# Kernel optimization log

Hardware: AMD Instinct MI355X
Metric: run time of the kernel (lower is better)

Reference implementation:

```python
import jax, jax.numpy as jnp
import numpy as np

DPITCH_RANGE = 24.0
SCALE = 1.0


def setup_inputs() -> dict:
    key = jax.random.key(0)
    ks = jax.random.split(key, 10)
    B, T, ND, SD, H = 512, 1024, 64, 3, 256
    inp_size = ND + SD  # 67
    w = lambda k, shape: (jax.random.normal(k, shape, jnp.float32) * 0.05)
    return {
        "noise": jax.random.normal(ks[0], (B, T, ND), jnp.float32),
        "gap_duration": jax.random.uniform(ks[1], (B, T + 1, SD - 1), dtype=jnp.float32),
        "W_ih": w(ks[2], (4 * H, inp_size)),
        "W_hh": w(ks[3], (4 * H, H)),
        "b_ih": w(ks[4], (4 * H,)),
        "b_hh": w(ks[5], (4 * H,)),
        "W1": w(ks[6], (H, H)),
        "b1": w(ks[7], (H,)),
        "W2": w(ks[8], (1, H)),
        "b2": w(ks[9], (1,)),
    }


def reference(noise, gap_duration, W_ih, W_hh, b_ih, b_hh, W1, b1, W2, b2):
    B, T, _ = noise.shape
    H = W_hh.shape[1]

    def head(out):  # Linear -> Tanh -> Linear -> Tanh, scaled to deltapitch
        hdn = jnp.tanh(out @ W1.T + b1)
        return jnp.tanh(hdn @ W2.T + b2) * (DPITCH_RANGE * SCALE)

    def lstm_cell(h, c, x):  # torch LSTM gate order: i, f, g, o
        gates = x @ W_ih.T + b_ih + h @ W_hh.T + b_hh
        i, f, g, o = jnp.split(gates, 4, axis=-1)
        c = jax.nn.sigmoid(f) * c + jax.nn.sigmoid(i) * jnp.tanh(g)
        h = jax.nn.sigmoid(o) * jnp.tanh(c)
        return h, c

    def step(carry, inp):
        out, h, c = carry
        n_t, gap_t = inp  # [B, ND], [B, SD-1]
        x = jnp.concatenate([gap_t, head(out)], axis=-1)  # [B, SD]
        h, c = lstm_cell(h, c, jnp.concatenate([x, n_t], axis=-1))
        return (h, h, c), x

    z = jnp.zeros((B, H), noise.dtype)
    (out, _, _), xs = jax.lax.scan(
        step, (z, z, z),
        (noise.transpose(1, 0, 2), gap_duration[:, :T].transpose(1, 0, 2)))
    x_last = jnp.concatenate([gap_duration[:, T], head(out)], axis=-1)
    return jnp.concatenate([xs.transpose(1, 0, 2), x_last[:, None, :]], axis=1)
```

## Files before the change

### kernel.cpp

```cpp
#include <hip/hip_runtime.h>
#include <stdint.h>
#include <stddef.h>

typedef __bf16 bf16x8 __attribute__((ext_vector_type(8)));
typedef float f32x4 __attribute__((ext_vector_type(4)));

#define MFMA16(a, b, c) __builtin_amdgcn_mfma_f32_16x16x32_bf16((a), (b), (c), 0, 0, 0)

#define TSTEPS 1024
#define NDIM   64
#define NKC    10
#define NGT    64
#define MB     16
#define GROUPS 32
#define SLICES 8

#define GOFF    ((size_t)0)
#define GBYTES  ((size_t)NGT * NKC * 1024)
#define W1OFF   (GOFF + GBYTES)
#define W1BYTES ((size_t)16 * 8 * 1024)
#define BOFF    (W1OFF + W1BYTES)
#define XOFF    (BOFF + 4096)
#define IDSB    ((size_t)1024)
#define PAYB    ((size_t)256 * 2 * 512 * 4)
#define WSNEED  (XOFF + IDSB + 2 * PAYB)

__device__ __forceinline__ uint16_t f2bf(float f) {
    union { float f; uint32_t u; } v; v.f = f;
    return (uint16_t)((v.u + 0x7FFFu + ((v.u >> 16) & 1u)) >> 16);
}
__device__ __forceinline__ float fsig(float x) { return 1.0f / (1.0f + __expf(-x)); }
__device__ __forceinline__ float ftanh(float x) { return 2.0f / (1.0f + __expf(-2.0f * x)) - 1.0f; }

__device__ __forceinline__ void bar_lgkm() {
    asm volatile("s_waitcnt lgkmcnt(0)" ::: "memory");
    __builtin_amdgcn_s_barrier();
    asm volatile("" ::: "memory");
}

#define FPOLL7(R0, R1, R2, R3, R4, R5, R6, O0, O1, O2, O3, O4, O5, O6, SB)   \
    asm volatile(                                                            \
        "global_load_dword %0, %7, %14 sc0\n\t"                              \
        "global_load_dword %1, %8, %14 sc0\n\t"                              \
        "global_load_dword %2, %9, %14 sc0\n\t"                              \
        "global_load_dword %3, %10, %14 sc0\n\t"                             \
        "global_load_dword %4, %11, %14 sc0\n\t"                             \
        "global_load_dword %5, %12, %14 sc0\n\t"                             \
        "global_load_dword %6, %13, %14 sc0\n\t"                             \
        "s_waitcnt vmcnt(0)"                                                 \
        : "=&v"(R0), "=&v"(R1), "=&v"(R2), "=&v"(R3),                        \
          "=&v"(R4), "=&v"(R5), "=&v"(R6)                                    \
        : "v"(O0), "v"(O1), "v"(O2), "v"(O3), "v"(O4), "v"(O5), "v"(O6),     \
          "s"(SB)                                                            \
        : "memory")

__global__ void prep_gates(const float* __restrict__ W_ih, const float* __restrict__ W_hh,
                           char* __restrict__ ws) {
    int F = blockIdx.x;
    int T = F / NKC, kc = F - T * NKC;
    int l = threadIdx.x;
    int row  = 16 * T + (l & 15);
    int unit = row >> 2, gt = row & 3;
    int orig = gt * 256 + unit;
    uint32_t w[4];
#pragma unroll
    for (int p = 0; p < 4; ++p) {
        float v[2];
#pragma unroll
        for (int e = 0; e < 2; ++e) {
            int k = 32 * kc + 8 * (l >> 4) + 2 * p + e;
            v[e] = (k < 64) ? W_ih[orig * 67 + 3 + k] : W_hh[orig * 256 + (k - 64)];
        }
        w[p] = (uint32_t)f2bf(v[0]) | ((uint32_t)f2bf(v[1]) << 16);
    }
    *(uint4*)(ws + GOFF + (size_t)F * 1024 + (size_t)l * 16) = make_uint4(w[0], w[1], w[2], w[3]);
}

__global__ void prep_w1(const float* __restrict__ W1, char* __restrict__ ws) {
    int F = blockIdx.x;
    int T = F / 8, kc = F - T * 8;
    int l = threadIdx.x;
    int row = 16 * T + (l & 15);
    uint32_t w[4];
#pragma unroll
    for (int p = 0; p < 4; ++p) {
        int k = 32 * kc + 8 * (l >> 4) + 2 * p;
        w[p] = (uint32_t)f2bf(W1[row * 256 + k]) | ((uint32_t)f2bf(W1[row * 256 + k + 1]) << 16);
    }
    *(uint4*)(ws + W1OFF + (size_t)F * 1024 + (size_t)l * 16) = make_uint4(w[0], w[1], w[2], w[3]);
}

__global__ void prep_small(const float* __restrict__ b_ih, const float* __restrict__ b_hh,
                           char* __restrict__ ws) {
    int t = threadIdx.x;
    float* sb = (float*)(ws + BOFF);
    if (t < 1024) {
        int unit = t >> 2, gt = t & 3;
        int orig = gt * 256 + unit;
        sb[t] = b_ih[orig] + b_hh[orig];
    }
}

__global__ __launch_bounds__(512, 2) void lstm_main(
        const float* __restrict__ noise, const float* __restrict__ gap,
        const float* __restrict__ W_ih, const float* __restrict__ b1p,
        const float* __restrict__ W2p, const float* __restrict__ b2p,
        char* __restrict__ ws, float* __restrict__ out) {
    __shared__ uint16_t act[MB * 320];
    __shared__ float dp_part[16][9];
    __shared__ float gxy[2][16][2];
    __shared__ int s_gf;

    const int tid  = threadIdx.x;
    const int w    = tid >> 6;
    const int lane = tid & 63;
    const int q    = lane >> 4;
    const int col  = lane & 15;
    const int g    = blockIdx.x >> 3;
    const int s    = blockIdx.x & 7;
    const int b0   = g * MB;
    const int swz  = (col & 7) << 3;

    const uint4* gfr  = (const uint4*)(ws + GOFF);
    const uint4* w1fr = (const uint4*)(ws + W1OFF);
    const float* bias = (const float*)(ws + BOFF);
    uint32_t* ids = (uint32_t*)(ws + XOFF);
    const uint64_t payF_base = (uint64_t)(uintptr_t)(ws + XOFF + IDSB);
    uint32_t* payS = (uint32_t*)(ws + XOFF + IDSB + PAYB);

    for (int i = tid; i < MB * 320; i += 512) act[i] = 0;

    const int T = 8 * s + w;
    uint4 gw[NKC];
#pragma unroll
    for (int kc = 0; kc < NKC; ++kc) gw[kc] = gfr[(size_t)(T * NKC + kc) * 64 + lane];
    uint4 w1w[16];
#pragma unroll
    for (int i = 0; i < 2; ++i)
#pragma unroll
        for (int kc = 0; kc < 8; ++kc)
            w1w[i * 8 + kc] = w1fr[(size_t)((2 * w + i) * 8 + kc) * 64 + lane];

    const int rb = 16 * T + 4 * q;
    const float bI = bias[rb], bF = bias[rb + 1], bG = bias[rb + 2], bO = bias[rb + 3];
    float wx0[4], wx1[4], wx2[4];
#pragma unroll
    for (int r = 0; r < 4; ++r) {
        int row = rb + r;
        int orig = (row & 3) * 256 + (row >> 2);
        wx0[r] = W_ih[orig * 67 + 0];
        wx1[r] = W_ih[orig * 67 + 1];
        wx2[r] = W_ih[orig * 67 + 2] * 24.0f;
    }
    float b1r[8], w2r[8];
#pragma unroll
    for (int a = 0; a < 2; ++a)
#pragma unroll
        for (int r = 0; r < 4; ++r) {
            int row = 32 * w + 16 * a + 4 * q + r;
            b1r[4 * a + r] = b1p[row];
            w2r[4 * a + r] = W2p[row];
        }
    const float b2v = b2p[0];

    const int myidx = g * 8 + s;
    const int myunit = 32 * s + 4 * w + q;

    uint32_t myx;
    asm volatile("s_getreg_b32 %0, hwreg(HW_REG_XCC_ID)" : "=s"(myx));
    if (tid == 0)
        __hip_atomic_store(&ids[myidx], 0x100u | (myx & 0xffu),
                           __ATOMIC_RELAXED, __HIP_MEMORY_SCOPE_AGENT);
    if (tid < 8) {
        uint32_t v;
        do { v = __hip_atomic_load(&ids[g * 8 + tid], __ATOMIC_RELAXED,
                                   __HIP_MEMORY_SCOPE_AGENT); } while (!(v & 0x100u));
        unsigned long long bal = __ballot((v & 0xffu) == (myx & 0xffu));
        if (tid == 0) s_gf = ((bal & 0xffull) == 0xffull) ? 1 : 0;
    }

    uint32_t vofB[7];
#pragma unroll
    for (int pi = 0; pi < 7; ++pi) {
        int p = (s + 1 + pi) & 7;
        vofB[pi] = ((uint32_t)(g * 8 + p) << 12) + (uint32_t)((64 * w + lane) * 4);
    }
    const uint32_t myvof = ((uint32_t)myidx << 12) + (uint32_t)((64 * w + lane) * 4);

    const int nbr = tid >> 5, nj = (tid & 31) * 2;
    const float* nptr = noise + (size_t)(b0 + nbr) * TSTEPS * NDIM + nj;
    float2 npf = *(const float2*)nptr;
    const bool xlead = (w == 7 && lane < 16);
    const bool olead = (s == 0 && w == 0);
    float2 gpf = make_float2(0.f, 0.f);
    if (xlead) gpf = *(const float2*)(gap + (size_t)(b0 + col) * (TSTEPS + 1) * 2);

    float creg = 0.f;
    float o_g0 = 0.f, o_g1 = 0.f, o_tdp = 0.f;
    const f32x4 fz = {0.f, 0.f, 0.f, 0.f};

    __syncthreads();
    bool fm = (s_gf != 0);

#pragma unroll 1
    for (int t = 0; t <= TSTEPS; ++t) {
        const int par = t & 1;
        const uint32_t tg = (uint32_t)t;

        if (t < TSTEPS) {
            uint32_t nv = (uint32_t)f2bf(npf.x) | ((uint32_t)f2bf(npf.y) << 16);
            int sw = (nbr & 7) << 3;
            *(uint32_t*)&act[nbr * 320 + (nj ^ sw)] = nv;
        }
        if (xlead) { gxy[par][col][0] = gpf.x; gxy[par][col][1] = gpf.y; }

        if (t > 0) {
            unsigned pend = 0x7f;
            if (fm) {
                int spins = 0;
                const uint32_t pb = (uint32_t)(par << 11);
                uint32_t o0 = vofB[0] + pb, o1 = vofB[1] + pb, o2 = vofB[2] + pb,
                         o3 = vofB[3] + pb, o4 = vofB[4] + pb, o5 = vofB[5] + pb,
                         o6 = vofB[6] + pb;
                for (;;) {
                    uint32_t r0, r1, r2, r3, r4, r5, r6;
                    FPOLL7(r0, r1, r2, r3, r4, r5, r6, o0, o1, o2, o3, o4, o5, o6,
                           payF_base);
                    uint32_t rr[7] = {r0, r1, r2, r3, r4, r5, r6};
#pragma unroll
                    for (int pi = 0; pi < 7; ++pi)
                        if ((pend & (1u << pi)) && (rr[pi] >> 16) == tg) {
                            int p = (s + 1 + pi) & 7;
                            int u = 32 * p + 4 * w + q;
                            act[col * 320 + ((64 + u) ^ swz)] = (uint16_t)rr[pi];
                            pend &= ~(1u << pi);
                        }
                    if (!pend) break;
                    if (++spins > 1000) { fm = false; break; }
                }
            }
            if (pend) {
                uint32_t vv[7];
                do {
#pragma unroll
                    for (int pi = 0; pi < 7; ++pi)
                        if (pend & (1u << pi)) {
                            int p = (s + 1 + pi) & 7;
                            vv[pi] = __hip_atomic_load(
                                &payS[(((g * 8 + p) * 2 + par) << 9) + 64 * w + lane],
                                __ATOMIC_RELAXED, __HIP_MEMORY_SCOPE_AGENT);
                        }
#pragma unroll
                    for (int pi = 0; pi < 7; ++pi)
                        if ((pend & (1u << pi)) && (vv[pi] >> 16) == tg) {
                            int p = (s + 1 + pi) & 7;
                            int u = 32 * p + 4 * w + q;
                            act[col * 320 + ((64 + u) ^ swz)] = (uint16_t)vv[pi];
                            pend &= ~(1u << pi);
                        }
                } while (pend);
            }
            fm = __all(fm);
            if (olead && q == 0) {
                float* o = out + ((size_t)(b0 + col) * (TSTEPS + 1) + (t - 1)) * 3;
                o[0] = o_g0; o[1] = o_g1; o[2] = 24.0f * o_tdp;
            }
        }
        if (t + 1 < TSTEPS) npf = *(const float2*)(nptr + (size_t)(t + 1) * NDIM);
        if (xlead && t < TSTEPS)
            gpf = *(const float2*)(gap + ((size_t)(b0 + col) * (TSTEPS + 1) + (t + 1)) * 2);
        bar_lgkm();

        f32x4 h0 = fz, h1 = fz, ga = fz;
        {
            bf16x8 bn0 = *(const bf16x8*)&act[col * 320 + ((8 * q) ^ swz)];
            bf16x8 bn1 = *(const bf16x8*)&act[col * 320 + ((32 + 8 * q) ^ swz)];
            ga = MFMA16(__builtin_bit_cast(bf16x8, gw[0]), bn0, ga);
            ga = MFMA16(__builtin_bit_cast(bf16x8, gw[1]), bn1, ga);
        }
#pragma unroll
        for (int kc = 0; kc < 8; ++kc) {
            bf16x8 bv = *(const bf16x8*)&act[col * 320 + ((64 + 32 * kc + 8 * q) ^ swz)];
            ga = MFMA16(__builtin_bit_cast(bf16x8, gw[2 + kc]), bv, ga);
            h0 = MFMA16(__builtin_bit_cast(bf16x8, w1w[kc]),     bv, h0);
            h1 = MFMA16(__builtin_bit_cast(bf16x8, w1w[8 + kc]), bv, h1);
        }
        float part = 0.f;
#pragma unroll
        for (int r = 0; r < 4; ++r) {
            part += ftanh(h0[r] + b1r[r])     * w2r[r];
            part += ftanh(h1[r] + b1r[4 + r]) * w2r[4 + r];
        }
        part += __shfl_xor(part, 16);
        part += __shfl_xor(part, 32);
        if (q == 0) dp_part[col][w] = part;
        bar_lgkm();

        const float* dpp = &dp_part[col][0];
        float inner = b2v + ((dpp[0] + dpp[1]) + (dpp[2] + dpp[3]))
                          + ((dpp[4] + dpp[5]) + (dpp[6] + dpp[7]));
        float tdp = ftanh(inner);
        const float g0 = gxy[par][col][0], g1 = gxy[par][col][1];
        o_g0 = g0; o_g1 = g1; o_tdp = tdp;

        if (t == TSTEPS) {
            if (olead && q == 0) {
                float* o = out + ((size_t)(b0 + col) * (TSTEPS + 1) + t) * 3;
                o[0] = g0; o[1] = g1; o[2] = 24.0f * tdp;
            }
            break;
        }

        float ii = ga[0] + bI + wx0[0] * g0 + wx1[0] * g1 + wx2[0] * tdp;
        float ff = ga[1] + bF + wx0[1] * g0 + wx1[1] * g1 + wx2[1] * tdp;
        float gg = ga[2] + bG + wx0[2] * g0 + wx1[2] * g1 + wx2[2] * tdp;
        float oo = ga[3] + bO + wx0[3] * g0 + wx1[3] * g1 + wx2[3] * tdp;
        float cn = fsig(ff) * creg + fsig(ii) * ftanh(gg);
        creg = cn;
        float hv = fsig(oo) * ftanh(cn);
        uint16_t hb = f2bf(hv);

        uint32_t word = ((uint32_t)(t + 1) << 16) | (uint32_t)hb;
        uint32_t wvo = myvof + (uint32_t)(((t + 1) & 1) << 11);
        asm volatile("global_store_dword %0, %1, %2 sc0"
                     :: "v"(wvo), "v"(word), "s"(payF_base) : "memory");
        __hip_atomic_store(&payS[((myidx * 2 + ((t + 1) & 1)) << 9) + 64 * w + lane],
                           word, __ATOMIC_RELAXED, __HIP_MEMORY_SCOPE_AGENT);
        act[col * 320 + ((64 + myunit) ^ swz)] = hb;
    }
}

extern "C" void kernel_launch(void* const* d_in, const int* in_sizes, int n_in,
                              void* d_out, int out_size, void* d_ws, size_t ws_size,
                              hipStream_t stream) {
    (void)in_sizes; (void)n_in; (void)out_size;
    if (ws_size < WSNEED) return;

    const float* noise = (const float*)d_in[0];
    const float* gap   = (const float*)d_in[1];
    const float* W_ih  = (const float*)d_in[2];
    const float* W_hh  = (const float*)d_in[3];
    const float* b_ih  = (const float*)d_in[4];
    const float* b_hh  = (const float*)d_in[5];
    const float* W1    = (const float*)d_in[6];
    const float* b1    = (const float*)d_in[7];
    const float* W2    = (const float*)d_in[8];
    const float* b2    = (const float*)d_in[9];
    char*  ws  = (char*)d_ws;
    float* out = (float*)d_out;

    hipMemsetAsync(ws + XOFF, 0, IDSB + 2 * PAYB, stream);
    hipLaunchKernelGGL(prep_gates, dim3(NGT * NKC), dim3(64), 0, stream, W_ih, W_hh, ws);
    hipLaunchKernelGGL(prep_w1,    dim3(16 * 8),    dim3(64), 0, stream, W1, ws);
    hipLaunchKernelGGL(prep_small, dim3(1), dim3(1024), 0, stream, b_ih, b_hh, ws);
    hipLaunchKernelGGL(lstm_main,  dim3(GROUPS * SLICES), dim3(512), 0, stream,
                       noise, gap, W_ih, b1, W2, b2, ws, out);
}
```

Baseline: 3.097 ms.

## Assign batch groups and slices by XCC so cooperating blocks share a die

Every block now publishes its XCC id and reads all 256 ids. It then derives its group and slice itself, so that whole 8-block groups are placed on one XCC wherever possible and can use the fast same-die polling path. Previously a group got the fast path only if the hardware scheduler happened to put all 8 blocks on one XCC. The fast-path poll also checks the slow payload buffer every 128 spins and falls back only after repeated misses, rather than after a fixed spin count. The cost is an all-block handshake at startup, and the scheme requires all 256 blocks to be co-resident, or the handshake deadlocks.

```diff
diff --git a/kernel.cpp b/kernel.cpp
--- a/kernel.cpp
+++ b/kernel.cpp
@@ -109,16 +109,13 @@
     __shared__ uint16_t act[MB * 320];
     __shared__ float dp_part[16][9];
     __shared__ float gxy[2][16][2];
-    __shared__ int s_gf;
+    __shared__ uint32_t sIds[256];
 
     const int tid  = threadIdx.x;
     const int w    = tid >> 6;
     const int lane = tid & 63;
     const int q    = lane >> 4;
     const int col  = lane & 15;
-    const int g    = blockIdx.x >> 3;
-    const int s    = blockIdx.x & 7;
-    const int b0   = g * MB;
     const int swz  = (col & 7) << 3;
 
     const uint4* gfr  = (const uint4*)(ws + GOFF);
@@ -130,6 +127,42 @@
 
     for (int i = tid; i < MB * 320; i += 512) act[i] = 0;
 
+    uint32_t myx;
+    asm volatile("s_getreg_b32 %0, hwreg(HW_REG_XCC_ID)" : "=s"(myx));
+    myx &= 0xffu;
+    if (tid == 0)
+        __hip_atomic_store(&ids[blockIdx.x], 0x100u | myx,
+                           __ATOMIC_RELAXED, __HIP_MEMORY_SCOPE_AGENT);
+    if (tid < 256) {
+        uint32_t v;
+        do { v = __hip_atomic_load(&ids[tid], __ATOMIC_RELAXED,
+                                   __HIP_MEMORY_SCOPE_AGENT); } while (!(v & 0x100u));
+        sIds[tid] = v & 0xffu;
+    }
+    __syncthreads();
+
+    const int myblk = blockIdx.x;
+    int cnt[8] = {0, 0, 0, 0, 0, 0, 0, 0};
+    int r = 0;
+    for (int j = 0; j < 256; ++j) {
+        int x = (int)sIds[j];
+        if (j < myblk && x == (int)myx) ++r;
+        ++cnt[x & 7];
+    }
+    int base = 0, NF = 0, Lpre = 0;
+    for (int x = 0; x < 8; ++x) {
+        int nf = cnt[x] >> 3;
+        if (x < (int)myx) { base += nf; Lpre += cnt[x] & 7; }
+        NF += nf;
+    }
+    const int nfm = cnt[myx & 7] >> 3;
+    int g, s; bool fast;
+    if (r < 8 * nfm) { g = base + (r >> 3); s = r & 7; fast = true; }
+    else { int L = Lpre + (r - 8 * nfm); g = NF + (L >> 3); s = L & 7; fast = false; }
+    const int b0 = g * MB;
+    const int myidx = g * 8 + s;
+    const int myunit = 32 * s + 4 * w + q;
+
     const int T = 8 * s + w;
     uint4 gw[NKC];
 #pragma unroll
@@ -145,45 +178,29 @@
     const float bI = bias[rb], bF = bias[rb + 1], bG = bias[rb + 2], bO = bias[rb + 3];
     float wx0[4], wx1[4], wx2[4];
 #pragma unroll
-    for (int r = 0; r < 4; ++r) {
-        int row = rb + r;
+    for (int rr = 0; rr < 4; ++rr) {
+        int row = rb + rr;
         int orig = (row & 3) * 256 + (row >> 2);
-        wx0[r] = W_ih[orig * 67 + 0];
-        wx1[r] = W_ih[orig * 67 + 1];
-        wx2[r] = W_ih[orig * 67 + 2] * 24.0f;
+        wx0[rr] = W_ih[orig * 67 + 0];
+        wx1[rr] = W_ih[orig * 67 + 1];
+        wx2[rr] = W_ih[orig * 67 + 2] * 24.0f;
     }
     float b1r[8], w2r[8];
 #pragma unroll
     for (int a = 0; a < 2; ++a)
 #pragma unroll
-        for (int r = 0; r < 4; ++r) {
-            int row = 32 * w + 16 * a + 4 * q + r;
-            b1r[4 * a + r] = b1p[row];
-            w2r[4 * a + r] = W2p[row];
+        for (int rr = 0; rr < 4; ++rr) {
+            int row = 32 * w + 16 * a + 4 * q + rr;
+            b1r[4 * a + rr] = b1p[row];
+            w2r[4 * a + rr] = W2p[row];
         }
     const float b2v = b2p[0];
 
-    const int myidx = g * 8 + s;
-    const int myunit = 32 * s + 4 * w + q;
-
-    uint32_t myx;
-    asm volatile("s_getreg_b32 %0, hwreg(HW_REG_XCC_ID)" : "=s"(myx));
-    if (tid == 0)
-        __hip_atomic_store(&ids[myidx], 0x100u | (myx & 0xffu),
-                           __ATOMIC_RELAXED, __HIP_MEMORY_SCOPE_AGENT);
-    if (tid < 8) {
-        uint32_t v;
-        do { v = __hip_atomic_load(&ids[g * 8 + tid], __ATOMIC_RELAXED,
-                                   __HIP_MEMORY_SCOPE_AGENT); } while (!(v & 0x100u));
-        unsigned long long bal = __ballot((v & 0xffu) == (myx & 0xffu));
-        if (tid == 0) s_gf = ((bal & 0xffull) == 0xffull) ? 1 : 0;
-    }
-
-    uint32_t vofB[7];
+    uint32_t vof[7];
 #pragma unroll
     for (int pi = 0; pi < 7; ++pi) {
         int p = (s + 1 + pi) & 7;
-        vofB[pi] = ((uint32_t)(g * 8 + p) << 12) + (uint32_t)((64 * w + lane) * 4);
+        vof[pi] = ((uint32_t)(g * 8 + p) << 12) + (uint32_t)((64 * w + lane) * 4);
     }
     const uint32_t myvof = ((uint32_t)myidx << 12) + (uint32_t)((64 * w + lane) * 4);
 
@@ -198,9 +215,10 @@
     float creg = 0.f;
     float o_g0 = 0.f, o_g1 = 0.f, o_tdp = 0.f;
     const f32x4 fz = {0.f, 0.f, 0.f, 0.f};
+    int fmMiss = 0;
+    bool fm = fast;
 
     __syncthreads();
-    bool fm = (s_gf != 0);
 
 #pragma unroll 1
     for (int t = 0; t <= TSTEPS; ++t) {
@@ -217,11 +235,11 @@
         if (t > 0) {
             unsigned pend = 0x7f;
             if (fm) {
+                const uint32_t parb = (uint32_t)(par << 11);
+                uint32_t o0 = vof[0] + parb, o1 = vof[1] + parb, o2 = vof[2] + parb,
+                         o3 = vof[3] + parb, o4 = vof[4] + parb, o5 = vof[5] + parb,
+                         o6 = vof[6] + parb;
                 int spins = 0;
-                const uint32_t pb = (uint32_t)(par << 11);
-                uint32_t o0 = vofB[0] + pb, o1 = vofB[1] + pb, o2 = vofB[2] + pb,
-                         o3 = vofB[3] + pb, o4 = vofB[4] + pb, o5 = vofB[5] + pb,
-                         o6 = vofB[6] + pb;
                 for (;;) {
                     uint32_t r0, r1, r2, r3, r4, r5, r6;
                     FPOLL7(r0, r1, r2, r3, r4, r5, r6, o0, o1, o2, o3, o4, o5, o6,
@@ -236,8 +254,28 @@
                             pend &= ~(1u << pi);
                         }
                     if (!pend) break;
-                    if (++spins > 1000) { fm = false; break; }
+                    if ((++spins & 127) == 127) {
+                        uint32_t vv[7];
+#pragma unroll
+                        for (int pi = 0; pi < 7; ++pi)
+                            if (pend & (1u << pi)) {
+                                int p = (s + 1 + pi) & 7;
+                                vv[pi] = __hip_atomic_load(
+                                    &payS[(((g * 8 + p) * 2 + par) << 9) + 64 * w + lane],
+                                    __ATOMIC_RELAXED, __HIP_MEMORY_SCOPE_AGENT);
+                            }
+#pragma unroll
+                        for (int pi = 0; pi < 7; ++pi)
+                            if ((pend & (1u << pi)) && (vv[pi] >> 16) == tg) {
+                                int p = (s + 1 + pi) & 7;
+                                int u = 32 * p + 4 * w + q;
+                                act[col * 320 + ((64 + u) ^ swz)] = (uint16_t)vv[pi];
+                                pend &= ~(1u << pi);
+                            }
+                        if (!pend) { ++fmMiss; break; }
+                    }
                 }
+                if (fmMiss >= 4) fm = false;
             }
             if (pend) {
                 uint32_t vv[7];
@@ -287,9 +325,9 @@
         }
         float part = 0.f;
 #pragma unroll
-        for (int r = 0; r < 4; ++r) {
-            part += ftanh(h0[r] + b1r[r])     * w2r[r];
-            part += ftanh(h1[r] + b1r[4 + r]) * w2r[4 + r];
+        for (int rr = 0; rr < 4; ++rr) {
+            part += ftanh(h0[rr] + b1r[rr])     * w2r[rr];
+            part += ftanh(h1[rr] + b1r[4 + rr]) * w2r[4 + rr];
         }
         part += __shfl_xor(part, 16);
         part += __shfl_xor(part, 32);
@@ -353,6 +391,6 @@
     hipLaunchKernelGGL(prep_gates, dim3(NGT * NKC), dim3(64), 0, stream, W_ih, W_hh, ws);
     hipLaunchKernelGGL(prep_w1,    dim3(16 * 8),    dim3(64), 0, stream, W1, ws);
     hipLaunchKernelGGL(prep_small, dim3(1), dim3(1024), 0, stream, b_ih, b_hh, ws);
-    hipLaunchKernelGGL(lstm_main,  dim3(GROUPS * SLICES), dim3(512), 0, stream,
+    hipLaunchKernelGGL(lstm_main,  dim3(256), dim3(512), 0, stream,
                        noise, gap, W_ih, b1, W2, b2, ws, out);
 }
```

Result: faster. 3.026 ms (-2.3%).
